# Kernel tuning notes

Hardware: AMD Instinct MI355X
Metric: run time of the kernel (lower is better)

The kernel has to match this reference:

```python
import jax, jax.numpy as jnp
import numpy as np

B, S, F = 4, 2048, 256
H, D = 8, 32            # n_heads, width_embedding; H*D == F
LN_EPS = 1e-3           # tf.keras LayerNormalization default epsilon


def setup_inputs() -> dict:
    key = jax.random.key(0)
    ks = jax.random.split(key, 6)
    s = 1.0 / np.sqrt(F)
    return {
        "x": jax.random.normal(ks[0], (B, S, F), dtype=jnp.float32),
        "Wq": jax.random.normal(ks[1], (F, H * D), dtype=jnp.float32) * s,
        "Wk": jax.random.normal(ks[2], (F, H * D), dtype=jnp.float32) * s,
        "Wv": jax.random.normal(ks[3], (F, H * D), dtype=jnp.float32) * s,
        "Wf": jax.random.normal(ks[4], (H * D, F), dtype=jnp.float32) * s,
        "bf": jnp.zeros((F,), dtype=jnp.float32),
    }


def reference(x, Wq, Wk, Wv, Wf, bf):
    # QKV projections (no bias), split heads: [B,S,H*D] -> [B,H,S,D]
    def split(t):
        return t.reshape(B, S, H, D).transpose(0, 2, 1, 3)

    q = split(x @ Wq) / jnp.sqrt(jnp.asarray(H, x.dtype))  # NOTE: module scales by sqrt(n_heads)
    k = split(x @ Wk)
    v = split(x @ Wv)

    scores = jnp.einsum("bhsd,bhtd->bhst", q, k)          # [B,H,S,S]
    attn = jax.nn.softmax(scores, axis=-1)
    ctx = jnp.einsum("bhst,bhtd->bhsd", attn, v)           # [B,H,S,D]

    y = ctx.transpose(0, 2, 1, 3).reshape(B, S, H * D)     # merge heads
    y = jax.nn.relu(y @ Wf + bf)                            # final dense with relu

    # residual + LayerNorm(center=False, scale=False)
    z = x + y
    mean = jnp.mean(z, axis=-1, keepdims=True)
    var = jnp.var(z, axis=-1, keepdims=True)
    return (z - mean) * jax.lax.rsqrt(var + LN_EPS)
```

## Files before the change

kernel.cpp:

```cpp
#include <hip/hip_runtime.h>
#include <math.h>

#define NB 4
#define NS 2048
#define NF 256
#define NH 8
#define ND 32

constexpr float LN_EPS = 1e-3f;
constexpr float QSCALE = 0.35355339059327373f;
constexpr float LOG2E  = 1.4426950408889634f;
constexpr int   NSPLIT = 2;
constexpr int   KRANGE = NS / NSPLIT;
constexpr size_t PO_PER = (size_t)NB * NH * NS * ND;

typedef __bf16 bf16x8 __attribute__((ext_vector_type(8)));
typedef float f32x4 __attribute__((ext_vector_type(4)));

__global__ __launch_bounds__(256)
void prep_w(const float* __restrict__ Wq, const float* __restrict__ Wk,
            const float* __restrict__ Wv, const float* __restrict__ Wf,
            unsigned short* __restrict__ wt)
{
    __shared__ float tile[64][65];
    const int wid = blockIdx.x;
    const int t = threadIdx.x;
    const int z = wid >> 4;
    const int tl = wid & 15;
    const float* W = (z == 0) ? Wq : (z == 1) ? Wk : (z == 2) ? Wv : Wf;
    const float scale = (z == 0) ? QSCALE * LOG2E : 1.0f;
    const int r0 = (tl >> 2) * 64, c0 = (tl & 3) * 64;
    const int tr = t >> 4, tc4 = (t & 15) * 4;

    #pragma unroll
    for (int p = 0; p < 4; ++p) {
        float4 v = *(const float4*)(W + (size_t)(r0 + tr + p * 16) * NF + c0 + tc4);
        tile[tr + p * 16][tc4 + 0] = v.x;
        tile[tr + p * 16][tc4 + 1] = v.y;
        tile[tr + p * 16][tc4 + 2] = v.z;
        tile[tr + p * 16][tc4 + 3] = v.w;
    }
    __syncthreads();
    #pragma unroll
    for (int p = 0; p < 4; ++p) {
        union { ushort4 u; __bf16 h[4]; } o;
        #pragma unroll
        for (int j = 0; j < 4; ++j)
            o.h[j] = (__bf16)(tile[tc4 + j][tr + p * 16] * scale);
        *(ushort4*)(wt + (size_t)z * 65536 + (size_t)(c0 + tr + p * 16) * NF + r0 + tc4) = o.u;
    }
}

__global__ __launch_bounds__(256)
void qkv_mfma(const float* __restrict__ x, const unsigned short* __restrict__ wt,
              unsigned short* __restrict__ qo, unsigned short* __restrict__ ko,
              unsigned short* __restrict__ vo)
{
    const int z = blockIdx.y;
    unsigned short* out = (z == 0) ? qo : (z == 1) ? ko : vo;
    const unsigned short* W = wt + (size_t)z * 65536;

    const int r0 = blockIdx.x * 64;
    const int t = threadIdx.x;
    const int w = t >> 6, lane = t & 63;
    const int l15 = lane & 15, lhi = lane >> 4;
    const int wr = w >> 1, wc = w & 1;

    f32x4 acc[2][8] = {};

    #pragma unroll 2
    for (int kt = 0; kt < NF; kt += 32) {
        const float* xr0 = x + (size_t)(r0 + wr * 32 + l15) * NF + kt + lhi * 8;
        const float* xr1 = x + (size_t)(r0 + wr * 32 + 16 + l15) * NF + kt + lhi * 8;
        float4 f00 = *(const float4*)xr0;
        float4 f01 = *(const float4*)(xr0 + 4);
        float4 f10 = *(const float4*)xr1;
        float4 f11 = *(const float4*)(xr1 + 4);
        bf16x8 a0, a1;
        a0[0] = (__bf16)f00.x; a0[1] = (__bf16)f00.y; a0[2] = (__bf16)f00.z; a0[3] = (__bf16)f00.w;
        a0[4] = (__bf16)f01.x; a0[5] = (__bf16)f01.y; a0[6] = (__bf16)f01.z; a0[7] = (__bf16)f01.w;
        a1[0] = (__bf16)f10.x; a1[1] = (__bf16)f10.y; a1[2] = (__bf16)f10.z; a1[3] = (__bf16)f10.w;
        a1[4] = (__bf16)f11.x; a1[5] = (__bf16)f11.y; a1[6] = (__bf16)f11.z; a1[7] = (__bf16)f11.w;
        #pragma unroll
        for (int c = 0; c < 8; ++c) {
            bf16x8 b = *(const bf16x8*)(W + (size_t)(wc * 128 + c * 16 + l15) * NF + kt + lhi * 8);
            acc[0][c] = __builtin_amdgcn_mfma_f32_16x16x32_bf16(a0, b, acc[0][c], 0, 0, 0);
            acc[1][c] = __builtin_amdgcn_mfma_f32_16x16x32_bf16(a1, b, acc[1][c], 0, 0, 0);
        }
    }

    #pragma unroll
    for (int i = 0; i < 2; ++i) {
        #pragma unroll
        for (int c = 0; c < 8; ++c) {
            const int col = wc * 128 + c * 16 + l15;
            const int h = col >> 5, d = col & 31;
            const int rowbase = r0 + wr * 32 + i * 16 + lhi * 4;
            const int b = rowbase >> 11, s = rowbase & 2047;
            if (z == 2) {
                union { ushort4 u; __bf16 h4[4]; } o;
                #pragma unroll
                for (int r = 0; r < 4; ++r) o.h4[r] = (__bf16)acc[i][c][r];
                *(ushort4*)(out + ((size_t)(b * NH + h) * ND + d) * NS + s) = o.u;
            } else {
                #pragma unroll
                for (int r = 0; r < 4; ++r) {
                    __bf16 o = (__bf16)acc[i][c][r];
                    out[((size_t)(b * NH + h) * NS + (s + r)) * ND + d] = *(unsigned short*)&o;
                }
            }
        }
    }
}

__global__ __launch_bounds__(256)
void attn_mfma(const unsigned short* __restrict__ q, const unsigned short* __restrict__ k,
               const unsigned short* __restrict__ v, float* __restrict__ po,
               float* __restrict__ pl)
{
    const int bh = blockIdx.x;
    const int s0 = blockIdx.y * 128;
    const int sp = blockIdx.z;
    const int kbase = sp * KRANGE;
    const int t = threadIdx.x;
    const int w = t >> 6;
    const int lane = t & 63;
    const int l15 = lane & 15;
    const int lhi = lane >> 4;
    const int sx  = l15 & 8;
    const int vd  = w * 8 + (lane >> 3);
    const int vk  = (lane & 7) * 8;
    const int vsx = vd & 8;

    __shared__ unsigned short vt[2][32][72];

    const unsigned short* qb  = q + (size_t)bh * NS * ND;
    const unsigned short* kb  = k + (size_t)bh * NS * ND;
    const unsigned short* vtg = v + (size_t)bh * ND * NS + (size_t)vd * NS;

    const int krow = (l15 >> 2) * 8 + (l15 & 3);
    const unsigned short* kbp = kb + (size_t)krow * ND + lhi * 8;

    bf16x8 qf0 = *(const bf16x8*)(qb + (size_t)(s0 + w * 32 + l15) * ND + lhi * 8);
    bf16x8 qf1 = *(const bf16x8*)(qb + (size_t)(s0 + w * 32 + 16 + l15) * ND + lhi * 8);

    float lp0 = 0.f, lp1 = 0.f;
    f32x4 acc00 = {0.f,0.f,0.f,0.f}, acc01 = {0.f,0.f,0.f,0.f};
    f32x4 acc10 = {0.f,0.f,0.f,0.f}, acc11 = {0.f,0.f,0.f,0.f};

    bf16x8 kf[4];
    kf[0] = *(const bf16x8*)(kbp + (size_t)kbase * ND);
    kf[1] = *(const bf16x8*)(kbp + (size_t)kbase * ND + 128);
    kf[2] = *(const bf16x8*)(kbp + (size_t)kbase * ND + 1024);
    kf[3] = *(const bf16x8*)(kbp + (size_t)kbase * ND + 1152);
    {
        bf16x8 vv = *(const bf16x8*)(vtg + kbase + vk);
        *(bf16x8*)&vt[0][vd][vk ^ vsx] = vv;
    }
    __syncthreads();

    int cur = 0;
    #pragma unroll 2
    for (int tI = 0; tI < 16; ++tI) {
        const int ktn = kbase + ((tI + 1) & 15) * 64;
        bf16x8 vvn = *(const bf16x8*)(vtg + ktn + vk);
        bf16x8 kn[4];
        kn[0] = *(const bf16x8*)(kbp + (size_t)ktn * ND);
        kn[1] = *(const bf16x8*)(kbp + (size_t)ktn * ND + 128);
        kn[2] = *(const bf16x8*)(kbp + (size_t)ktn * ND + 1024);
        kn[3] = *(const bf16x8*)(kbp + (size_t)ktn * ND + 1152);

        const f32x4 zero = {0.f, 0.f, 0.f, 0.f};
        f32x4 sc0[4], sc1[4];
        __builtin_amdgcn_s_setprio(1);
        #pragma unroll
        for (int f = 0; f < 4; ++f) {
            sc0[f] = __builtin_amdgcn_mfma_f32_16x16x32_bf16(kf[f], qf0, zero, 0, 0, 0);
            sc1[f] = __builtin_amdgcn_mfma_f32_16x16x32_bf16(kf[f], qf1, zero, 0, 0, 0);
        }
        __builtin_amdgcn_s_setprio(0);

        bf16x8 pa00, pa01, pa10, pa11;
        float a0 = 0.f, a1 = 0.f;
        #pragma unroll
        for (int r = 0; r < 4; ++r) {
            float p0 = __builtin_amdgcn_exp2f(sc0[0][r]);
            float p1 = __builtin_amdgcn_exp2f(sc0[1][r]);
            float p2 = __builtin_amdgcn_exp2f(sc0[2][r]);
            float p3 = __builtin_amdgcn_exp2f(sc0[3][r]);
            pa00[r]     = (__bf16)p0;
            pa00[4 + r] = (__bf16)p1;
            pa01[r]     = (__bf16)p2;
            pa01[4 + r] = (__bf16)p3;
            a0 += (p0 + p1) + (p2 + p3);
            float s0_ = __builtin_amdgcn_exp2f(sc1[0][r]);
            float s1_ = __builtin_amdgcn_exp2f(sc1[1][r]);
            float s2_ = __builtin_amdgcn_exp2f(sc1[2][r]);
            float s3_ = __builtin_amdgcn_exp2f(sc1[3][r]);
            pa10[r]     = (__bf16)s0_;
            pa10[4 + r] = (__bf16)s1_;
            pa11[r]     = (__bf16)s2_;
            pa11[4 + r] = (__bf16)s3_;
            a1 += (s0_ + s1_) + (s2_ + s3_);
        }
        lp0 += a0; lp1 += a1;

        const int co0 = (lhi * 8) ^ sx;
        const int co1 = (32 + lhi * 8) ^ sx;
        bf16x8 vfa0 = *(const bf16x8*)&vt[cur][l15][co0];
        bf16x8 vfb0 = *(const bf16x8*)&vt[cur][16 + l15][co0];
        bf16x8 vfa1 = *(const bf16x8*)&vt[cur][l15][co1];
        bf16x8 vfb1 = *(const bf16x8*)&vt[cur][16 + l15][co1];
        __builtin_amdgcn_s_setprio(1);
        acc00 = __builtin_amdgcn_mfma_f32_16x16x32_bf16(pa00, vfa0, acc00, 0, 0, 0);
        acc01 = __builtin_amdgcn_mfma_f32_16x16x32_bf16(pa00, vfb0, acc01, 0, 0, 0);
        acc10 = __builtin_amdgcn_mfma_f32_16x16x32_bf16(pa10, vfa0, acc10, 0, 0, 0);
        acc11 = __builtin_amdgcn_mfma_f32_16x16x32_bf16(pa10, vfb0, acc11, 0, 0, 0);
        acc00 = __builtin_amdgcn_mfma_f32_16x16x32_bf16(pa01, vfa1, acc00, 0, 0, 0);
        acc01 = __builtin_amdgcn_mfma_f32_16x16x32_bf16(pa01, vfb1, acc01, 0, 0, 0);
        acc10 = __builtin_amdgcn_mfma_f32_16x16x32_bf16(pa11, vfa1, acc10, 0, 0, 0);
        acc11 = __builtin_amdgcn_mfma_f32_16x16x32_bf16(pa11, vfb1, acc11, 0, 0, 0);
        __builtin_amdgcn_s_setprio(0);

        *(bf16x8*)&vt[cur ^ 1][vd][vk ^ vsx] = vvn;
        #pragma unroll
        for (int f = 0; f < 4; ++f) kf[f] = kn[f];
        __syncthreads();
        cur ^= 1;
    }

    lp0 += __shfl_xor(lp0, 16);
    lp0 += __shfl_xor(lp0, 32);
    lp1 += __shfl_xor(lp1, 16);
    lp1 += __shfl_xor(lp1, 32);

    float* pob = po + (size_t)sp * PO_PER;
    float* plb = pl + (size_t)sp * (NB * NH * NS);
    #pragma unroll
    for (int r = 0; r < 4; ++r) {
        float li0 = __shfl(lp0, lhi * 4 + r);
        float li1 = __shfl(lp1, lhi * 4 + r);
        int row0 = s0 + w * 32 + lhi * 4 + r;
        int row1 = row0 + 16;
        float* op0 = pob + ((size_t)bh * NS + row0) * ND;
        float* op1 = pob + ((size_t)bh * NS + row1) * ND;
        op0[l15]      = acc00[r];
        op0[16 + l15] = acc01[r];
        op1[l15]      = acc10[r];
        op1[16 + l15] = acc11[r];
        if (l15 == 0) {
            plb[bh * NS + row0] = li0;
            plb[bh * NS + row1] = li1;
        }
    }
}

__global__ __launch_bounds__(256)
void combine(const float* __restrict__ po, const float* __restrict__ pl,
             unsigned short* __restrict__ ctxb)
{
    const int idx = blockIdx.x * 256 + threadIdx.x;
    const int row = idx >> 2;
    const int dd = (idx & 3) * 8;
    const float* p0 = po + (size_t)row * ND + dd;
    const float* p1 = p0 + PO_PER;
    float inv = 1.0f / (pl[row] + pl[row + NB * NH * NS]);
    float4 a0 = *(const float4*)p0;
    float4 a1 = *(const float4*)(p0 + 4);
    float4 b0 = *(const float4*)p1;
    float4 b1 = *(const float4*)(p1 + 4);
    union { ushort4 u[2]; __bf16 h[8]; } o;
    o.h[0] = (__bf16)((a0.x + b0.x) * inv);
    o.h[1] = (__bf16)((a0.y + b0.y) * inv);
    o.h[2] = (__bf16)((a0.z + b0.z) * inv);
    o.h[3] = (__bf16)((a0.w + b0.w) * inv);
    o.h[4] = (__bf16)((a1.x + b1.x) * inv);
    o.h[5] = (__bf16)((a1.y + b1.y) * inv);
    o.h[6] = (__bf16)((a1.z + b1.z) * inv);
    o.h[7] = (__bf16)((a1.w + b1.w) * inv);
    const int bh = row >> 11, s = row & 2047;
    const int b = bh >> 3, h = bh & 7;
    unsigned short* op = ctxb + ((size_t)b * NS + s) * NF + h * ND + dd;
    *(ushort4*)op = o.u[0];
    *(ushort4*)(op + 4) = o.u[1];
}

__global__ __launch_bounds__(256)
void dense_ln(const unsigned short* __restrict__ ctxb, const unsigned short* __restrict__ wft,
              const float* __restrict__ bfp, const float* __restrict__ x,
              float* __restrict__ out)
{
    const int r0 = blockIdx.x * 32;
    const int t = threadIdx.x;
    const int w = t >> 6;
    const int lane = t & 63;
    const int l15 = lane & 15;
    const int lhi = lane >> 4;

    __shared__ float zs[32][258];

    f32x4 acc[2][4] = {};

    #pragma unroll 2
    for (int kt = 0; kt < NF; kt += 32) {
        bf16x8 a0 = *(const bf16x8*)(ctxb + (size_t)(r0 + l15) * NF + kt + lhi * 8);
        bf16x8 a1 = *(const bf16x8*)(ctxb + (size_t)(r0 + 16 + l15) * NF + kt + lhi * 8);
        #pragma unroll
        for (int c = 0; c < 4; ++c) {
            bf16x8 b = *(const bf16x8*)(wft + (size_t)(w * 64 + c * 16 + l15) * NF + kt + lhi * 8);
            acc[0][c] = __builtin_amdgcn_mfma_f32_16x16x32_bf16(a0, b, acc[0][c], 0, 0, 0);
            acc[1][c] = __builtin_amdgcn_mfma_f32_16x16x32_bf16(a1, b, acc[1][c], 0, 0, 0);
        }
    }

    #pragma unroll
    for (int i = 0; i < 2; ++i) {
        #pragma unroll
        for (int c = 0; c < 4; ++c) {
            const int col = w * 64 + c * 16 + l15;
            const float bb = bfp[col];
            #pragma unroll
            for (int r = 0; r < 4; ++r) {
                const int row = i * 16 + lhi * 4 + r;
                zs[row][col] = fmaxf(acc[i][c][r] + bb, 0.0f);
            }
        }
    }
    __syncthreads();

    #pragma unroll
    for (int i = 0; i < 8; ++i) {
        const int row = w * 8 + i;
        float4 yv = *(const float4*)&zs[row][lane * 4];
        float4 xv = *(const float4*)(x + (size_t)(r0 + row) * NF + lane * 4);
        float z0 = xv.x + yv.x, z1 = xv.y + yv.y;
        float z2 = xv.z + yv.z, z3 = xv.w + yv.w;
        float sum = z0 + z1 + z2 + z3;
        float sq  = z0*z0 + z1*z1 + z2*z2 + z3*z3;
        #pragma unroll
        for (int o = 1; o < 64; o <<= 1) {
            sum += __shfl_xor(sum, o);
            sq  += __shfl_xor(sq, o);
        }
        float mean = sum * (1.0f / NF);
        float var  = sq * (1.0f / NF) - mean * mean;
        float rstd = rsqrtf(var + LN_EPS);
        float4 o4;
        o4.x = (z0 - mean) * rstd;
        o4.y = (z1 - mean) * rstd;
        o4.z = (z2 - mean) * rstd;
        o4.w = (z3 - mean) * rstd;
        *(float4*)(out + (size_t)(r0 + row) * NF + lane * 4) = o4;
    }
}

extern "C" void kernel_launch(void* const* d_in, const int* in_sizes, int n_in,
                              void* d_out, int out_size, void* d_ws, size_t ws_size,
                              hipStream_t stream)
{
    const float* x  = (const float*)d_in[0];
    const float* Wq = (const float*)d_in[1];
    const float* Wk = (const float*)d_in[2];
    const float* Wv = (const float*)d_in[3];
    const float* Wf = (const float*)d_in[4];
    const float* bf = (const float*)d_in[5];
    float* out = (float*)d_out;

    const size_t per = (size_t)NB * NH * NS * ND;
    unsigned short* q    = (unsigned short*)d_ws;
    unsigned short* kk   = q + per;
    unsigned short* vv   = kk + per;
    unsigned short* wt   = vv + per;
    unsigned short* ctxb = wt + 4 * 65536;
    float* po = (float*)(ctxb + per);
    float* pl = po + (size_t)NSPLIT * PO_PER;

    prep_w<<<dim3(64), 256, 0, stream>>>(Wq, Wk, Wv, Wf, wt);
    qkv_mfma<<<dim3(128, 3), 256, 0, stream>>>(x, wt, q, kk, vv);
    attn_mfma<<<dim3(NB * NH, NS / 128, NSPLIT), 256, 0, stream>>>(q, kk, vv, po, pl);
    combine<<<dim3((NB * NS * NF / 8) / 256), 256, 0, stream>>>(po, pl, ctxb);
    dense_ln<<<dim3((NB * NS) / 32), 256, 0, stream>>>(ctxb, wt + 3 * 65536, bf, x, out);
}
```

Baseline: 81.89 us.

## Drop split-K attention and normalize directly into bf16 context buffer

Removes the two-way key split in the attention kernel, so each block walks all 2048 keys and writes normalized bf16 context straight into the merged-head layout. This eliminates the fp32 partial-output buffers and the separate combine kernel launch along with their global memory traffic. In exchange the attention grid halves to 512 blocks of 256 threads, which lowers parallelism and occupancy on a large GPU, and each block runs twice as long.

```diff
diff --git a/kernel.cpp b/kernel.cpp
--- a/kernel.cpp
+++ b/kernel.cpp
@@ -10,9 +10,6 @@
 constexpr float LN_EPS = 1e-3f;
 constexpr float QSCALE = 0.35355339059327373f;
 constexpr float LOG2E  = 1.4426950408889634f;
-constexpr int   NSPLIT = 2;
-constexpr int   KRANGE = NS / NSPLIT;
-constexpr size_t PO_PER = (size_t)NB * NH * NS * ND;
 
 typedef __bf16 bf16x8 __attribute__((ext_vector_type(8)));
 typedef float f32x4 __attribute__((ext_vector_type(4)));
@@ -115,13 +112,10 @@
 
 __global__ __launch_bounds__(256)
 void attn_mfma(const unsigned short* __restrict__ q, const unsigned short* __restrict__ k,
-               const unsigned short* __restrict__ v, float* __restrict__ po,
-               float* __restrict__ pl)
+               const unsigned short* __restrict__ v, unsigned short* __restrict__ ctxb)
 {
     const int bh = blockIdx.x;
     const int s0 = blockIdx.y * 128;
-    const int sp = blockIdx.z;
-    const int kbase = sp * KRANGE;
     const int t = threadIdx.x;
     const int w = t >> 6;
     const int lane = t & 63;
@@ -149,20 +143,20 @@
     f32x4 acc10 = {0.f,0.f,0.f,0.f}, acc11 = {0.f,0.f,0.f,0.f};
 
     bf16x8 kf[4];
-    kf[0] = *(const bf16x8*)(kbp + (size_t)kbase * ND);
-    kf[1] = *(const bf16x8*)(kbp + (size_t)kbase * ND + 128);
-    kf[2] = *(const bf16x8*)(kbp + (size_t)kbase * ND + 1024);
-    kf[3] = *(const bf16x8*)(kbp + (size_t)kbase * ND + 1152);
+    kf[0] = *(const bf16x8*)(kbp);
+    kf[1] = *(const bf16x8*)(kbp + 128);
+    kf[2] = *(const bf16x8*)(kbp + 1024);
+    kf[3] = *(const bf16x8*)(kbp + 1152);
     {
-        bf16x8 vv = *(const bf16x8*)(vtg + kbase + vk);
+        bf16x8 vv = *(const bf16x8*)(vtg + vk);
         *(bf16x8*)&vt[0][vd][vk ^ vsx] = vv;
     }
     __syncthreads();
 
     int cur = 0;
     #pragma unroll 2
-    for (int tI = 0; tI < 16; ++tI) {
-        const int ktn = kbase + ((tI + 1) & 15) * 64;
+    for (int tI = 0; tI < 32; ++tI) {
+        const int ktn = ((tI + 1) & 31) * 64;
         bf16x8 vvn = *(const bf16x8*)(vtg + ktn + vk);
         bf16x8 kn[4];
         kn[0] = *(const bf16x8*)(kbp + (size_t)ktn * ND);
@@ -234,55 +228,24 @@
     lp1 += __shfl_xor(lp1, 16);
     lp1 += __shfl_xor(lp1, 32);
 
-    float* pob = po + (size_t)sp * PO_PER;
-    float* plb = pl + (size_t)sp * (NB * NH * NS);
+    const int b = bh >> 3, h = bh & 7;
     #pragma unroll
     for (int r = 0; r < 4; ++r) {
-        float li0 = __shfl(lp0, lhi * 4 + r);
-        float li1 = __shfl(lp1, lhi * 4 + r);
+        float inv0 = 1.0f / __shfl(lp0, lhi * 4 + r);
+        float inv1 = 1.0f / __shfl(lp1, lhi * 4 + r);
         int row0 = s0 + w * 32 + lhi * 4 + r;
         int row1 = row0 + 16;
-        float* op0 = pob + ((size_t)bh * NS + row0) * ND;
-        float* op1 = pob + ((size_t)bh * NS + row1) * ND;
-        op0[l15]      = acc00[r];
-        op0[16 + l15] = acc01[r];
-        op1[l15]      = acc10[r];
-        op1[16 + l15] = acc11[r];
-        if (l15 == 0) {
-            plb[bh * NS + row0] = li0;
-            plb[bh * NS + row1] = li1;
-        }
-    }
-}
-
-__global__ __launch_bounds__(256)
-void combine(const float* __restrict__ po, const float* __restrict__ pl,
-             unsigned short* __restrict__ ctxb)
-{
-    const int idx = blockIdx.x * 256 + threadIdx.x;
-    const int row = idx >> 2;
-    const int dd = (idx & 3) * 8;
-    const float* p0 = po + (size_t)row * ND + dd;
-    const float* p1 = p0 + PO_PER;
-    float inv = 1.0f / (pl[row] + pl[row + NB * NH * NS]);
-    float4 a0 = *(const float4*)p0;
-    float4 a1 = *(const float4*)(p0 + 4);
-    float4 b0 = *(const float4*)p1;
-    float4 b1 = *(const float4*)(p1 + 4);
-    union { ushort4 u[2]; __bf16 h[8]; } o;
-    o.h[0] = (__bf16)((a0.x + b0.x) * inv);
-    o.h[1] = (__bf16)((a0.y + b0.y) * inv);
-    o.h[2] = (__bf16)((a0.z + b0.z) * inv);
-    o.h[3] = (__bf16)((a0.w + b0.w) * inv);
-    o.h[4] = (__bf16)((a1.x + b1.x) * inv);
-    o.h[5] = (__bf16)((a1.y + b1.y) * inv);
-    o.h[6] = (__bf16)((a1.z + b1.z) * inv);
-    o.h[7] = (__bf16)((a1.w + b1.w) * inv);
-    const int bh = row >> 11, s = row & 2047;
-    const int b = bh >> 3, h = bh & 7;
-    unsigned short* op = ctxb + ((size_t)b * NS + s) * NF + h * ND + dd;
-    *(ushort4*)op = o.u[0];
-    *(ushort4*)(op + 4) = o.u[1];
+        unsigned short* op0 = ctxb + ((size_t)b * NS + row0) * NF + h * ND;
+        unsigned short* op1 = ctxb + ((size_t)b * NS + row1) * NF + h * ND;
+        __bf16 o00 = (__bf16)(acc00[r] * inv0);
+        __bf16 o01 = (__bf16)(acc01[r] * inv0);
+        __bf16 o10 = (__bf16)(acc10[r] * inv1);
+        __bf16 o11 = (__bf16)(acc11[r] * inv1);
+        op0[l15]      = *(unsigned short*)&o00;
+        op0[16 + l15] = *(unsigned short*)&o01;
+        op1[l15]      = *(unsigned short*)&o10;
+        op1[16 + l15] = *(unsigned short*)&o11;
+    }
 }
 
 __global__ __launch_bounds__(256)
@@ -372,12 +335,9 @@
     unsigned short* vv   = kk + per;
     unsigned short* wt   = vv + per;
     unsigned short* ctxb = wt + 4 * 65536;
-    float* po = (float*)(ctxb + per);
-    float* pl = po + (size_t)NSPLIT * PO_PER;
 
     prep_w<<<dim3(64), 256, 0, stream>>>(Wq, Wk, Wv, Wf, wt);
     qkv_mfma<<<dim3(128, 3), 256, 0, stream>>>(x, wt, q, kk, vv);
-    attn_mfma<<<dim3(NB * NH, NS / 128, NSPLIT), 256, 0, stream>>>(q, kk, vv, po, pl);
-    combine<<<dim3((NB * NS * NF / 8) / 256), 256, 0, stream>>>(po, pl, ctxb);
+    attn_mfma<<<dim3(NB * NH, NS / 128), 256, 0, stream>>>(q, kk, vv, ctxb);
     dense_ln<<<dim3((NB * NS) / 32), 256, 0, stream>>>(ctxb, wt + 3 * 65536, bf, x, out);
 }
```

New measurement: 77.13 us. 5.8% less time.
